# Optimization experiments

Measured on AMD Instinct MI355X. Metric: run time of the kernel, lower is better.

## Reference

```python
import jax, jax.numpy as jnp
import numpy as np

D_MODEL = 384; N_LAYER = 8; N_MELS = 80; D_STATE = 16; EXPAND = 2; D_CONV = 4
D_INNER = EXPAND * D_MODEL           # 768
DT_RANK = (D_MODEL + 15) // 16       # 24 ('auto')
B = 4; L = 512


def setup_inputs() -> dict:
    key = jax.random.key(0)
    ks = jax.random.split(key, 12)
    g = lambda k, shape, s=0.02: jax.random.normal(k, shape, dtype=jnp.float32) * s
    A_log = jnp.tile(jnp.log(jnp.arange(1, D_STATE + 1, dtype=jnp.float32))[None, None, :],
                     (N_LAYER, D_INNER, 1))
    return {
        "x": jax.random.normal(ks[0], (B, L, N_MELS), dtype=jnp.float32),
        "enc_output": jax.random.normal(ks[1], (B, L, D_MODEL), dtype=jnp.float32),
        "w_in": g(ks[2], (N_MELS, D_MODEL)),
        "b_in": jnp.zeros((D_MODEL,), jnp.float32),
        "ln_w": jnp.ones((N_LAYER, D_MODEL), jnp.float32),
        "inproj_w": g(ks[3], (N_LAYER, D_MODEL, 2 * D_INNER)),
        "conv_w": g(ks[4], (N_LAYER, D_INNER, D_CONV), 0.1),
        "conv_b": jnp.zeros((N_LAYER, D_INNER), jnp.float32),
        "xproj_w": g(ks[5], (N_LAYER, D_INNER, DT_RANK + 2 * D_STATE)),
        "dtproj_w": g(ks[6], (N_LAYER, DT_RANK, D_INNER), 0.1),
        "dtproj_b": g(ks[7], (N_LAYER, D_INNER), 0.1),
        "A_log": A_log,
        "D": jnp.ones((N_LAYER, D_INNER), jnp.float32),
        "outproj_w": g(ks[8], (N_LAYER, D_INNER, D_MODEL)),
        "normf_w": jnp.ones((D_MODEL,), jnp.float32),
        "w_out": g(ks[9], (D_MODEL, N_MELS)),
    }


def rmsnorm(x, w, eps=1e-5):
    return x * jax.lax.rsqrt(jnp.mean(x * x, axis=-1, keepdims=True) + eps) * w


def selective_scan(u, delta, A, Bm, Cm, Dp):
    # u, delta: (b,l,d); A: (d,n); Bm, Cm: (b,l,n); Dp: (d,)
    dA = jnp.exp(jnp.einsum('bld,dn->bldn', delta, A))          # (b,l,d,n)
    dBu = jnp.einsum('bld,bln,bld->bldn', delta, Bm, u)          # (b,l,d,n)

    def step(h, xs):
        dA_t, dBu_t, C_t = xs                                    # (b,d,n),(b,d,n),(b,n)
        h = dA_t * h + dBu_t
        y = jnp.einsum('bdn,bn->bd', h, C_t)
        return h, y

    h0 = jnp.zeros((u.shape[0], u.shape[2], A.shape[1]), u.dtype)
    _, ys = jax.lax.scan(step, h0, (dA.transpose(1, 0, 2, 3),
                                    dBu.transpose(1, 0, 2, 3),
                                    Cm.transpose(1, 0, 2)))
    return ys.transpose(1, 0, 2) + u * Dp                        # (b,l,d)


def mamba_layer(x, ln, ip, cw, cb, xp, dw, db, al, dp, op):
    h = rmsnorm(x, ln)
    xr = h @ ip                                                  # (b,l,2*d_inner)
    xs, res = jnp.split(xr, 2, axis=-1)
    # depthwise causal conv1d: pad d_conv-1 on the left, truncate to L
    xc = jax.lax.conv_general_dilated(xs.transpose(0, 2, 1), cw[:, None, :],
                                      (1,), [(D_CONV - 1, 0)],
                                      feature_group_count=D_INNER)
    xs = jax.nn.silu((xc + cb[None, :, None]).transpose(0, 2, 1))
    xdbl = xs @ xp                                               # (b,l,dt_rank+2n)
    dt = xdbl[..., :DT_RANK]
    Bm = xdbl[..., DT_RANK:DT_RANK + D_STATE]
    Cm = xdbl[..., DT_RANK + D_STATE:]
    delta = jax.nn.softplus(dt @ dw + db)
    y = selective_scan(xs, delta, -jnp.exp(al), Bm, Cm, dp)
    y = y * jax.nn.silu(res)
    return x + y @ op


def reference(x, enc_output, w_in, b_in, ln_w, inproj_w, conv_w, conv_b,
              xproj_w, dtproj_w, dtproj_b, A_log, D, outproj_w, normf_w, w_out):
    h = x @ w_in + b_in
    half = N_LAYER // 2
    for i in range(half):
        h = mamba_layer(h, ln_w[i], inproj_w[i], conv_w[i], conv_b[i], xproj_w[i],
                        dtproj_w[i], dtproj_b[i], A_log[i], D[i], outproj_w[i])
    # soft attention: decoder states attend over encoder output
    scores = jnp.einsum('bqd,bkd->bqk', h, enc_output)
    h = jnp.einsum('bqk,bkd->bqd', jax.nn.softmax(scores, axis=-1), enc_output)
    for i in range(half, N_LAYER):
        h = mamba_layer(h, ln_w[i], inproj_w[i], conv_w[i], conv_b[i], xproj_w[i],
                        dtproj_w[i], dtproj_b[i], A_log[i], D[i], outproj_w[i])
    h = rmsnorm(h, normf_w)
    return h @ w_out
```

## Files before the change

### kernel.cpp

```cpp
#include <hip/hip_runtime.h>
#include <hip/hip_bf16.h>
#include <math.h>

#define D_MODEL 384
#define N_LAYER 8
#define N_MELS  80
#define D_STATE 16
#define D_CONV  4
#define D_INNER 768
#define DT_RANK 24
#define BB      4
#define LL      512
#define MTOK    (BB*LL)

#define BMt 64
#define BNt 64
#define BKt 16

#define XP_N   56
#define XPS    12
#define XPKC   64

typedef __attribute__((ext_vector_type(8))) short bf16x8;
typedef __attribute__((ext_vector_type(4))) short bf16x4;
typedef __attribute__((ext_vector_type(4))) float f32x4;

__device__ __forceinline__ float silu_f(float x) { return x / (1.f + __expf(-x)); }
__device__ __forceinline__ short bf_raw(float x) {
  __hip_bfloat16 h = __float2bfloat16(x);
  return *reinterpret_cast<short*>(&h);
}
__device__ __forceinline__ float bfu(unsigned short u) {
  unsigned v = ((unsigned)u) << 16;
  return *reinterpret_cast<float*>(&v);
}

template<int EPI>
__global__ __launch_bounds__(256) void gemm_f32(
    const float* __restrict__ A, int lda,
    const float* __restrict__ W, int ldw,
    const float* __restrict__ bias,
    float* __restrict__ C, int ldc,
    int M, int N, int K)
{
  __shared__ float As[BKt][BMt];
  __shared__ float Ws[BKt][BNt];
  const int tid = threadIdx.x;
  const int tx = tid & 15, ty = tid >> 4;
  const int m0 = blockIdx.y * BMt, n0 = blockIdx.x * BNt;
  const int am = tid >> 2, ak4 = (tid & 3) << 2;
  const int wk = tid >> 4, wn4 = (tid & 15) << 2;

  float acc[4][4] = {};

  for (int k0 = 0; k0 < K; k0 += BKt) {
    float4 va = make_float4(0.f, 0.f, 0.f, 0.f);
    {
      int m = m0 + am;
      if (m < M) {
        if (k0 + ak4 + 3 < K) {
          va = *reinterpret_cast<const float4*>(&A[(size_t)m * lda + k0 + ak4]);
        } else {
          float t[4];
          #pragma unroll
          for (int j = 0; j < 4; ++j)
            t[j] = (k0 + ak4 + j < K) ? A[(size_t)m * lda + k0 + ak4 + j] : 0.f;
          va = make_float4(t[0], t[1], t[2], t[3]);
        }
      }
    }
    As[ak4 + 0][am] = va.x;
    As[ak4 + 1][am] = va.y;
    As[ak4 + 2][am] = va.z;
    As[ak4 + 3][am] = va.w;

    float4 vw = make_float4(0.f, 0.f, 0.f, 0.f);
    {
      int kw = k0 + wk;
      if (kw < K) {
        if (n0 + wn4 + 3 < N) {
          vw = *reinterpret_cast<const float4*>(&W[(size_t)kw * ldw + n0 + wn4]);
        } else {
          float t[4];
          #pragma unroll
          for (int j = 0; j < 4; ++j)
            t[j] = (n0 + wn4 + j < N) ? W[(size_t)kw * ldw + n0 + wn4 + j] : 0.f;
          vw = make_float4(t[0], t[1], t[2], t[3]);
        }
      }
    }
    *reinterpret_cast<float4*>(&Ws[wk][wn4]) = vw;

    __syncthreads();
    #pragma unroll
    for (int kk = 0; kk < BKt; ++kk) {
      const float4 a4 = *reinterpret_cast<const float4*>(&As[kk][ty << 2]);
      const float4 w4 = *reinterpret_cast<const float4*>(&Ws[kk][tx << 2]);
      float av[4] = {a4.x, a4.y, a4.z, a4.w};
      float wv[4] = {w4.x, w4.y, w4.z, w4.w};
      #pragma unroll
      for (int i = 0; i < 4; ++i)
        #pragma unroll
        for (int j = 0; j < 4; ++j)
          acc[i][j] += av[i] * wv[j];
    }
    __syncthreads();
  }

  #pragma unroll
  for (int i = 0; i < 4; ++i) {
    int row = m0 + (ty << 2) + i;
    if (row >= M) continue;
    #pragma unroll
    for (int j = 0; j < 4; ++j) {
      int col = n0 + (tx << 2) + j;
      if (col >= N) continue;
      float v = acc[i][j];
      if (EPI == 1) v += bias[col];
      C[(size_t)row * ldc + col] = v;
    }
  }
}

template<int EPI, int OBF>
__global__ __launch_bounds__(256) void gemm_bf16(
    const __hip_bfloat16* __restrict__ A,
    const __hip_bfloat16* __restrict__ WT,
    const float* __restrict__ resid,
    float* __restrict__ C,
    __hip_bfloat16* __restrict__ Cb,
    int ldc, int M, int N, int K)
{
  __shared__ __align__(16) __hip_bfloat16 Asl[64][72];
  __shared__ __align__(16) __hip_bfloat16 Bsl[64][72];
  const int tid = threadIdx.x;
  const int wave = tid >> 6, lane = tid & 63;
  const int m0 = blockIdx.y * 64, n0 = blockIdx.x * 64;
  const int lrow = tid >> 2;
  const int lk   = (tid & 3) << 4;
  const int g16 = lane >> 4;
  const int l16 = lane & 15;

  f32x4 acc[4] = {};

  for (int k0 = 0; k0 < K; k0 += 64) {
    const uint4* ga = reinterpret_cast<const uint4*>(&A[(size_t)(m0 + lrow) * K + k0 + lk]);
    uint4* la = reinterpret_cast<uint4*>(&Asl[lrow][lk]);
    la[0] = ga[0]; la[1] = ga[1];
    const uint4* gb = reinterpret_cast<const uint4*>(&WT[(size_t)(n0 + lrow) * K + k0 + lk]);
    uint4* lb = reinterpret_cast<uint4*>(&Bsl[lrow][lk]);
    lb[0] = gb[0]; lb[1] = gb[1];
    __syncthreads();
    #pragma unroll
    for (int kk = 0; kk < 64; kk += 32) {
      bf16x8 a = *reinterpret_cast<const bf16x8*>(&Asl[wave * 16 + l16][kk + g16 * 8]);
      #pragma unroll
      for (int f = 0; f < 4; ++f) {
        bf16x8 b = *reinterpret_cast<const bf16x8*>(&Bsl[f * 16 + l16][kk + g16 * 8]);
        acc[f] = __builtin_amdgcn_mfma_f32_16x16x32_bf16(a, b, acc[f], 0, 0, 0);
      }
    }
    __syncthreads();
  }

  #pragma unroll
  for (int f = 0; f < 4; ++f) {
    #pragma unroll
    for (int r = 0; r < 4; ++r) {
      int row = m0 + wave * 16 + g16 * 4 + r;
      int col = n0 + f * 16 + l16;
      float v = acc[f][r];
      if (EPI == 3) v += resid[(size_t)row * ldc + col];
      if (OBF) Cb[(size_t)row * ldc + col] = __float2bfloat16(v);
      else     C[(size_t)row * ldc + col] = v;
    }
  }
}

__global__ __launch_bounds__(256) void gemm_bf16_bat(
    const __hip_bfloat16* __restrict__ A, size_t sA,
    const __hip_bfloat16* __restrict__ WT, size_t sW,
    float* __restrict__ C, size_t sC,
    int M, int N, int K)
{
  A  += (size_t)blockIdx.z * sA;
  WT += (size_t)blockIdx.z * sW;
  C  += (size_t)blockIdx.z * sC;
  __shared__ __align__(16) __hip_bfloat16 Asl[64][72];
  __shared__ __align__(16) __hip_bfloat16 Bsl[64][72];
  const int tid = threadIdx.x;
  const int wave = tid >> 6, lane = tid & 63;
  const int m0 = blockIdx.y * 64, n0 = blockIdx.x * 64;
  const int lrow = tid >> 2;
  const int lk   = (tid & 3) << 4;
  const int g16 = lane >> 4;
  const int l16 = lane & 15;

  f32x4 acc[4] = {};

  for (int k0 = 0; k0 < K; k0 += 64) {
    const uint4* ga = reinterpret_cast<const uint4*>(&A[(size_t)(m0 + lrow) * K + k0 + lk]);
    uint4* la = reinterpret_cast<uint4*>(&Asl[lrow][lk]);
    la[0] = ga[0]; la[1] = ga[1];
    const uint4* gb = reinterpret_cast<const uint4*>(&WT[(size_t)(n0 + lrow) * K + k0 + lk]);
    uint4* lb = reinterpret_cast<uint4*>(&Bsl[lrow][lk]);
    lb[0] = gb[0]; lb[1] = gb[1];
    __syncthreads();
    #pragma unroll
    for (int kk = 0; kk < 64; kk += 32) {
      bf16x8 a = *reinterpret_cast<const bf16x8*>(&Asl[wave * 16 + l16][kk + g16 * 8]);
      #pragma unroll
      for (int f = 0; f < 4; ++f) {
        bf16x8 b = *reinterpret_cast<const bf16x8*>(&Bsl[f * 16 + l16][kk + g16 * 8]);
        acc[f] = __builtin_amdgcn_mfma_f32_16x16x32_bf16(a, b, acc[f], 0, 0, 0);
      }
    }
    __syncthreads();
  }

  #pragma unroll
  for (int f = 0; f < 4; ++f) {
    #pragma unroll
    for (int r = 0; r < 4; ++r) {
      int row = m0 + wave * 16 + g16 * 4 + r;
      int col = n0 + f * 16 + l16;
      C[(size_t)row * N + col] = acc[f][r];
    }
  }
}

__global__ __launch_bounds__(256) void xproj_conv_splitk(
    const __hip_bfloat16* __restrict__ xrb,
    const float* __restrict__ cw,
    const float* __restrict__ cb,
    const __hip_bfloat16* __restrict__ WT,
    float* __restrict__ part)
{
  __shared__ __align__(16) __hip_bfloat16 Asl[64][72];
  __shared__ __align__(16) __hip_bfloat16 Bsl[64][72];
  const int tid = threadIdx.x;
  const int wave = tid >> 6, lane = tid & 63;
  const int split = blockIdx.x;
  const int m0 = blockIdx.y * 64;
  const int kbase = split * XPKC;
  const int lrow = tid >> 2;
  const int lk   = (tid & 3) << 4;
  const int g16 = lane >> 4;
  const int l16 = lane & 15;

  {
    const int m = m0 + lrow;
    const int b = m >> 9, l = m & 511;
    const int dcol0 = kbase + lk;
    unsigned wrow[4][8];
    #pragma unroll
    for (int k = 0; k < 4; ++k) {
      int t = l - 3 + k;
      if (t >= 0) {
        const uint4* p = reinterpret_cast<const uint4*>(
            &xrb[((size_t)(b * LL + t)) * (2 * D_INNER) + dcol0]);
        uint4 q0 = p[0], q1 = p[1];
        wrow[k][0] = q0.x; wrow[k][1] = q0.y; wrow[k][2] = q0.z; wrow[k][3] = q0.w;
        wrow[k][4] = q1.x; wrow[k][5] = q1.y; wrow[k][6] = q1.z; wrow[k][7] = q1.w;
      } else {
        #pragma unroll
        for (int w = 0; w < 8; ++w) wrow[k][w] = 0u;
      }
    }
    #pragma unroll
    for (int j = 0; j < 16; ++j) {
      float4 cw4 = *reinterpret_cast<const float4*>(&cw[(size_t)(dcol0 + j) * 4]);
      float cwa[4] = {cw4.x, cw4.y, cw4.z, cw4.w};
      float a = cb[dcol0 + j];
      #pragma unroll
      for (int k = 0; k < 4; ++k) {
        unsigned w = wrow[k][j >> 1];
        unsigned short hv = (j & 1) ? (unsigned short)(w >> 16) : (unsigned short)(w & 0xffff);
        a += bfu(hv) * cwa[k];
      }
      Asl[lrow][lk + j] = __float2bfloat16(silu_f(a));
    }
  }

  const uint4* gb = reinterpret_cast<const uint4*>(&WT[(size_t)lrow * D_INNER + kbase + lk]);
  uint4* lb = reinterpret_cast<uint4*>(&Bsl[lrow][lk]);
  lb[0] = gb[0]; lb[1] = gb[1];
  __syncthreads();

  f32x4 acc[4] = {};
  #pragma unroll
  for (int kk = 0; kk < 64; kk += 32) {
    bf16x8 a = *reinterpret_cast<const bf16x8*>(&Asl[wave * 16 + l16][kk + g16 * 8]);
    #pragma unroll
    for (int f = 0; f < 4; ++f) {
      bf16x8 b = *reinterpret_cast<const bf16x8*>(&Bsl[f * 16 + l16][kk + g16 * 8]);
      acc[f] = __builtin_amdgcn_mfma_f32_16x16x32_bf16(a, b, acc[f], 0, 0, 0);
    }
  }

  #pragma unroll
  for (int f = 0; f < 4; ++f) {
    #pragma unroll
    for (int r = 0; r < 4; ++r) {
      int row = m0 + wave * 16 + g16 * 4 + r;
      int col = f * 16 + l16;
      part[((size_t)split * MTOK + row) * 64 + col] = acc[f][r];
    }
  }
}

__global__ __launch_bounds__(256) void xproj_reduce_kernel(
    const float* __restrict__ part, float* __restrict__ xdbl)
{
  int idx = blockIdx.x * 256 + threadIdx.x;
  if (idx >= MTOK * XP_N) return;
  int m = idx / XP_N, col = idx - m * XP_N;
  float s = 0.f;
  #pragma unroll
  for (int p = 0; p < XPS; ++p)
    s += part[((size_t)p * MTOK + m) * 64 + col];
  xdbl[idx] = s;
}

__global__ __launch_bounds__(256) void wconv_t_kernel(
    const float* __restrict__ src, __hip_bfloat16* __restrict__ dst,
    int K, int N, size_t ldl)
{
  __shared__ float tile[32][33];
  int l = blockIdx.z;
  int kb = blockIdx.y * 32, nb = blockIdx.x * 32;
  int tn = threadIdx.x & 31, tk = threadIdx.x >> 5;
  const float* s = src + (size_t)l * K * N;
  __hip_bfloat16* dd = dst + (size_t)l * ldl;
  #pragma unroll
  for (int i = 0; i < 4; ++i) {
    int k = kb + tk + i * 8, n = nb + tn;
    tile[tk + i * 8][tn] = (k < K && n < N) ? s[(size_t)k * N + n] : 0.f;
  }
  __syncthreads();
  #pragma unroll
  for (int i = 0; i < 4; ++i) {
    int n = nb + tk + i * 8, k = kb + tn;
    if (n < N && k < K) dd[(size_t)n * K + k] = __float2bfloat16(tile[tn][tk + i * 8]);
  }
}

__global__ __launch_bounds__(256) void f2b_kernel(
    const float* __restrict__ src, __hip_bfloat16* __restrict__ dst, int n)
{
  int i = (blockIdx.x * 256 + threadIdx.x) * 4;
  if (i >= n) return;
  float4 v = *reinterpret_cast<const float4*>(&src[i]);
  bf16x4 o;
  o[0] = bf_raw(v.x); o[1] = bf_raw(v.y); o[2] = bf_raw(v.z); o[3] = bf_raw(v.w);
  *reinterpret_cast<bf16x4*>(&dst[i]) = o;
}

__global__ __launch_bounds__(256) void softmax_rows_kernel(
    const float* __restrict__ scores, __hip_bfloat16* __restrict__ P)
{
  int row = (blockIdx.x * 256 + threadIdx.x) >> 6;
  int lane = threadIdx.x & 63;
  if (row >= BB * LL) return;
  const float* s = scores + (size_t)row * LL + lane * 8;
  float4 v0 = *reinterpret_cast<const float4*>(s);
  float4 v1 = *reinterpret_cast<const float4*>(s + 4);
  float mx = fmaxf(fmaxf(fmaxf(v0.x, v0.y), fmaxf(v0.z, v0.w)),
                   fmaxf(fmaxf(v1.x, v1.y), fmaxf(v1.z, v1.w)));
  #pragma unroll
  for (int off = 32; off; off >>= 1) mx = fmaxf(mx, __shfl_xor(mx, off, 64));
  float e[8];
  e[0] = __expf(v0.x - mx); e[1] = __expf(v0.y - mx);
  e[2] = __expf(v0.z - mx); e[3] = __expf(v0.w - mx);
  e[4] = __expf(v1.x - mx); e[5] = __expf(v1.y - mx);
  e[6] = __expf(v1.z - mx); e[7] = __expf(v1.w - mx);
  float sum = ((e[0] + e[1]) + (e[2] + e[3])) + ((e[4] + e[5]) + (e[6] + e[7]));
  #pragma unroll
  for (int off = 32; off; off >>= 1) sum += __shfl_xor(sum, off, 64);
  float inv = 1.f / sum;
  bf16x8 o;
  #pragma unroll
  for (int j = 0; j < 8; ++j) o[j] = bf_raw(e[j] * inv);
  *reinterpret_cast<bf16x8*>(&P[(size_t)row * LL + lane * 8]) = o;
}

__global__ __launch_bounds__(256) void rmsnorm_kernel(
    const float* __restrict__ x, const float* __restrict__ w,
    float* __restrict__ out, __hip_bfloat16* __restrict__ outb, int M, int N)
{
  int gw = (blockIdx.x * blockDim.x + threadIdx.x) >> 6;
  int lane = threadIdx.x & 63;
  if (gw >= M) return;
  const float* row = x + (size_t)gw * N;
  float ss = 0.f;
  for (int j = lane; j < N; j += 64) { float v = row[j]; ss += v * v; }
  #pragma unroll
  for (int off = 32; off; off >>= 1) ss += __shfl_xor(ss, off, 64);
  float scale = rsqrtf(ss / (float)N + 1e-5f);
  float* orow = out ? out + (size_t)gw * N : nullptr;
  __hip_bfloat16* brow = outb + (size_t)gw * N;
  for (int j = lane; j < N; j += 64) {
    float v = row[j] * scale * w[j];
    if (orow) orow[j] = v;
    brow[j] = __float2bfloat16(v);
  }
}

#define SC6_T  16
#define SC6_NC 32
__global__ __launch_bounds__(512) void scan_kernel10(
    const __hip_bfloat16* __restrict__ xrb,
    const float* __restrict__ xdbl,
    const float* __restrict__ A_log,
    const float* __restrict__ Dp,
    const float* __restrict__ dtw,
    const float* __restrict__ dtb,
    const float* __restrict__ cw,
    const float* __restrict__ cb,
    __hip_bfloat16* __restrict__ yg)
{
  __shared__ float sdelta[2][LL];
  __shared__ unsigned supk[LL];
  __shared__ float sdw[2][DT_RANK];
  __shared__ float sP[2][SC6_NC][D_STATE + 1];
  __shared__ float sS[2][SC6_NC][D_STATE + 1];
  __shared__ float sH0[2][SC6_NC][D_STATE + 1];
  __shared__ float sY[2][LL][5];

  unsigned* sxr = reinterpret_cast<unsigned*>(&sY[0][0][0]);

  const int id = blockIdx.x;
  const int r  = id / 48;
  const int G  = id % 48;
  const int b  = G / 12;
  const int q  = G % 12;
  const int d0 = q * 64 + 2 * r;
  const int d1 = d0 + 1;

  const int tid = threadIdx.x;
  const int n = tid & 15;
  const int c = tid >> 4;

  if (tid < DT_RANK) {
    sdw[0][tid] = dtw[tid * D_INNER + d0];
    sdw[1][tid] = dtw[tid * D_INNER + d1];
  }
  if (tid < 3) sxr[tid] = 0u;
  __syncthreads();

  {
    const int l = tid;
    const size_t m = (size_t)(b * LL + l);
    float acc0 = dtb[d0], acc1 = dtb[d1];
    const float* xrow = &xdbl[m * 56];
    #pragma unroll
    for (int k4 = 0; k4 < DT_RANK; k4 += 4) {
      float4 xv = *reinterpret_cast<const float4*>(&xrow[k4]);
      acc0 += xv.x * sdw[0][k4] + xv.y * sdw[0][k4 + 1] + xv.z * sdw[0][k4 + 2] + xv.w * sdw[0][k4 + 3];
      acc1 += xv.x * sdw[1][k4] + xv.y * sdw[1][k4 + 1] + xv.z * sdw[1][k4 + 2] + xv.w * sdw[1][k4 + 3];
    }
    sdelta[0][l] = (acc0 > 20.f) ? acc0 : log1pf(__expf(acc0));
    sdelta[1][l] = (acc1 > 20.f) ? acc1 : log1pf(__expf(acc1));
    sxr[3 + l] = *reinterpret_cast<const unsigned*>(&xrb[m * (2 * D_INNER) + d0]);
  }
  __syncthreads();

  {
    const int l = tid;
    float4 cw0 = *reinterpret_cast<const float4*>(&cw[(size_t)d0 * 4]);
    float4 cw1 = *reinterpret_cast<const float4*>(&cw[(size_t)d1 * 4]);
    float cwa0[4] = {cw0.x, cw0.y, cw0.z, cw0.w};
    float cwa1[4] = {cw1.x, cw1.y, cw1.z, cw1.w};
    float u0 = cb[d0], u1 = cb[d1];
    #pragma unroll
    for (int k = 0; k < 4; ++k) {
      unsigned w = sxr[l + k];
      u0 += bfu((unsigned short)(w & 0xffff)) * cwa0[k];
      u1 += bfu((unsigned short)(w >> 16)) * cwa1[k];
    }
    unsigned pk = ((unsigned)(unsigned short)bf_raw(silu_f(u0))) |
                  (((unsigned)(unsigned short)bf_raw(silu_f(u1))) << 16);
    supk[l] = pk;
  }

  const float Aval0 = -__expf(A_log[d0 * D_STATE + n]);
  const float Aval1 = -__expf(A_log[d1 * D_STATE + n]);
  const int l0 = c * SC6_T;
  const size_t mbase = (size_t)(b * LL + l0);

  float Bv_s[SC6_T];
  #pragma unroll
  for (int t = 0; t < SC6_T; ++t)
    Bv_s[t] = xdbl[(mbase + t) * 56 + DT_RANK + n];

  __syncthreads();

  float a_s[2][SC6_T];
  {
    float P0 = 1.f, S0 = 0.f, P1 = 1.f, S1 = 0.f;
    #pragma unroll
    for (int t = 0; t < SC6_T; ++t) {
      int l = l0 + t;
      unsigned uu = supk[l];
      float uv0 = bfu((unsigned short)(uu & 0xffff));
      float uv1 = bfu((unsigned short)(uu >> 16));
      float dv0 = sdelta[0][l];
      float dv1 = sdelta[1][l];
      float a0 = __expf(dv0 * Aval0);
      float a1 = __expf(dv1 * Aval1);
      P0 *= a0; S0 = a0 * S0 + (dv0 * Bv_s[t]) * uv0;
      P1 *= a1; S1 = a1 * S1 + (dv1 * Bv_s[t]) * uv1;
      a_s[0][t] = a0; a_s[1][t] = a1;
    }
    sP[0][c][n] = P0; sS[0][c][n] = S0;
    sP[1][c][n] = P1; sS[1][c][n] = S1;
  }

  float Cv_s[SC6_T];
  #pragma unroll
  for (int t = 0; t < SC6_T; ++t)
    Cv_s[t] = xdbl[(mbase + t) * 56 + DT_RANK + D_STATE + n];

  __syncthreads();

  {
    const int c2 = tid & 31;
    const int n2 = tid >> 5;
    #pragma unroll
    for (int dd = 0; dd < 2; ++dd) {
      float p = sP[dd][c2][n2];
      float s = sS[dd][c2][n2];
      #pragma unroll
      for (int k = 1; k <= 16; k <<= 1) {
        float pp = __shfl_up(p, k, 64);
        float sp = __shfl_up(s, k, 64);
        if (c2 >= k) { s = p * sp + s; p = p * pp; }
      }
      if (c2 == 0) sH0[dd][0][n2] = 0.f;
      if (c2 < 31) sH0[dd][c2 + 1][n2] = s;
    }
  }
  __syncthreads();

  {
    float h0 = sH0[0][c][n];
    float h1 = sH0[1][c][n];
    #pragma unroll
    for (int t = 0; t < SC6_T; ++t) {
      int l = l0 + t;
      unsigned uu = supk[l];
      float uv0 = bfu((unsigned short)(uu & 0xffff));
      float uv1 = bfu((unsigned short)(uu >> 16));
      float dv0 = sdelta[0][l];
      float dv1 = sdelta[1][l];
      h0 = a_s[0][t] * h0 + (dv0 * Bv_s[t]) * uv0;
      h1 = a_s[1][t] * h1 + (dv1 * Bv_s[t]) * uv1;
      float c0 = h0 * Cv_s[t];
      float c1 = h1 * Cv_s[t];
      c0 += __shfl_xor(c0, 1, 64); c0 += __shfl_xor(c0, 2, 64);
      c1 += __shfl_xor(c1, 1, 64); c1 += __shfl_xor(c1, 2, 64);
      if ((n & 3) == 0) { sY[0][l][n >> 2] = c0; sY[1][l][n >> 2] = c1; }
    }
  }
  __syncthreads();

  {
    const int l = tid;
    const size_t m = (size_t)(b * LL + l);
    unsigned uu = supk[l];
    float uv0 = bfu((unsigned short)(uu & 0xffff));
    float uv1 = bfu((unsigned short)(uu >> 16));
    float y0 = (sY[0][l][0] + sY[0][l][1]) + (sY[0][l][2] + sY[0][l][3]) + uv0 * Dp[d0];
    float y1 = (sY[1][l][0] + sY[1][l][1]) + (sY[1][l][2] + sY[1][l][3]) + uv1 * Dp[d1];
    unsigned rr = *reinterpret_cast<const unsigned*>(&xrb[m * (2 * D_INNER) + D_INNER + d0]);
    float r0 = bfu((unsigned short)(rr & 0xffff));
    float r1 = bfu((unsigned short)(rr >> 16));
    y0 *= silu_f(r0);
    y1 *= silu_f(r1);
    unsigned outw = ((unsigned)(unsigned short)bf_raw(y0)) |
                    (((unsigned)(unsigned short)bf_raw(y1)) << 16);
    *reinterpret_cast<unsigned*>(&yg[m * D_INNER + d0]) = outw;
  }
}

extern "C" void kernel_launch(void* const* d_in, const int* in_sizes, int n_in,
                              void* d_out, int out_size, void* d_ws, size_t ws_size,
                              hipStream_t stream) {
  const float* x        = (const float*)d_in[0];
  const float* enc      = (const float*)d_in[1];
  const float* w_in     = (const float*)d_in[2];
  const float* b_in     = (const float*)d_in[3];
  const float* ln_w     = (const float*)d_in[4];
  const float* inproj_w = (const float*)d_in[5];
  const float* conv_w   = (const float*)d_in[6];
  const float* conv_b   = (const float*)d_in[7];
  const float* xproj_w  = (const float*)d_in[8];
  const float* dtproj_w = (const float*)d_in[9];
  const float* dtproj_b = (const float*)d_in[10];
  const float* A_log    = (const float*)d_in[11];
  const float* Dvec     = (const float*)d_in[12];
  const float* outproj_w= (const float*)d_in[13];
  const float* normf_w  = (const float*)d_in[14];
  const float* w_out    = (const float*)d_in[15];

  float* ws = (float*)d_ws;
  float* h     = ws; ws += MTOK * D_MODEL;
  float* hn    = ws; ws += MTOK * D_MODEL;
  float* xdbl  = ws; ws += MTOK * XP_N;
  float* xpart = ws; ws += XPS * MTOK * 64;
  float* h2    = ws; ws += MTOK * D_MODEL;
  float* scores= ws; ws += BB * LL * LL;
  __hip_bfloat16* xr_bf = (__hip_bfloat16*)ws; ws += MTOK * 2 * D_INNER / 2;
  __hip_bfloat16* hn_bf = (__hip_bfloat16*)ws; ws += MTOK * D_MODEL / 2;
  __hip_bfloat16* yg_bf = (__hip_bfloat16*)ws; ws += MTOK * D_INNER / 2;
  __hip_bfloat16* h_bf  = (__hip_bfloat16*)ws; ws += MTOK * D_MODEL / 2;
  __hip_bfloat16* P_bf  = (__hip_bfloat16*)ws; ws += BB * LL * LL / 2;
  __hip_bfloat16* enc_bf= (__hip_bfloat16*)ws; ws += BB * LL * D_MODEL / 2;
  __hip_bfloat16* encT  = (__hip_bfloat16*)ws; ws += BB * LL * D_MODEL / 2;
  __hip_bfloat16* WinT  = (__hip_bfloat16*)ws; ws += N_LAYER * D_MODEL * 2 * D_INNER / 2;
  __hip_bfloat16* WoutT = (__hip_bfloat16*)ws; ws += N_LAYER * D_INNER * D_MODEL / 2;
  __hip_bfloat16* XpT   = (__hip_bfloat16*)ws; ws += N_LAYER * 64 * D_INNER / 2;

  dim3 blk256(256), blk512(512);

  wconv_t_kernel<<<dim3(2 * D_INNER / 32, D_MODEL / 32, N_LAYER), blk256, 0, stream>>>(
      inproj_w, WinT, D_MODEL, 2 * D_INNER, (size_t)2 * D_INNER * D_MODEL);
  wconv_t_kernel<<<dim3(D_MODEL / 32, D_INNER / 32, N_LAYER), blk256, 0, stream>>>(
      outproj_w, WoutT, D_INNER, D_MODEL, (size_t)D_MODEL * D_INNER);
  wconv_t_kernel<<<dim3((XP_N + 31) / 32, D_INNER / 32, N_LAYER), blk256, 0, stream>>>(
      xproj_w, XpT, D_INNER, XP_N, (size_t)64 * D_INNER);
  f2b_kernel<<<(BB * LL * D_MODEL / 4 + 255) / 256, blk256, 0, stream>>>(
      enc, enc_bf, BB * LL * D_MODEL);
  wconv_t_kernel<<<dim3(D_MODEL / 32, LL / 32, BB), blk256, 0, stream>>>(
      enc, encT, LL, D_MODEL, (size_t)D_MODEL * LL);

  gemm_f32<1><<<dim3(D_MODEL / BNt, MTOK / BMt), blk256, 0, stream>>>(
      x, N_MELS, w_in, D_MODEL, b_in, h, D_MODEL, MTOK, D_MODEL, N_MELS);

  auto mamba = [&](float* hcur, int i) {
    rmsnorm_kernel<<<MTOK * 64 / 256, blk256, 0, stream>>>(
        hcur, ln_w + (size_t)i * D_MODEL, nullptr, hn_bf, MTOK, D_MODEL);
    gemm_bf16<0, 1><<<dim3(2 * D_INNER / 64, MTOK / 64), blk256, 0, stream>>>(
        hn_bf, WinT + (size_t)i * D_MODEL * 2 * D_INNER, nullptr,
        nullptr, xr_bf, 2 * D_INNER, MTOK, 2 * D_INNER, D_MODEL);
    xproj_conv_splitk<<<dim3(XPS, MTOK / 64), blk256, 0, stream>>>(
        xr_bf, conv_w + (size_t)i * D_INNER * D_CONV, conv_b + (size_t)i * D_INNER,
        XpT + (size_t)i * 64 * D_INNER, xpart);
    xproj_reduce_kernel<<<(MTOK * XP_N + 255) / 256, blk256, 0, stream>>>(xpart, xdbl);
    scan_kernel10<<<BB * D_INNER / 2, blk512, 0, stream>>>(
        xr_bf, xdbl, A_log + (size_t)i * D_INNER * D_STATE, Dvec + (size_t)i * D_INNER,
        dtproj_w + (size_t)i * DT_RANK * D_INNER, dtproj_b + (size_t)i * D_INNER,
        conv_w + (size_t)i * D_INNER * D_CONV, conv_b + (size_t)i * D_INNER,
        yg_bf);
    gemm_bf16<3, 0><<<dim3(D_MODEL / 64, MTOK / 64), blk256, 0, stream>>>(
        yg_bf, WoutT + (size_t)i * D_INNER * D_MODEL, hcur,
        hcur, nullptr, D_MODEL, MTOK, D_MODEL, D_INNER);
  };

  for (int i = 0; i < N_LAYER / 2; ++i) mamba(h, i);

  f2b_kernel<<<(MTOK * D_MODEL / 4 + 255) / 256, blk256, 0, stream>>>(
      h, h_bf, MTOK * D_MODEL);
  gemm_bf16_bat<<<dim3(LL / 64, LL / 64, BB), blk256, 0, stream>>>(
      h_bf, (size_t)LL * D_MODEL, enc_bf, (size_t)LL * D_MODEL,
      scores, (size_t)LL * LL, LL, LL, D_MODEL);
  softmax_rows_kernel<<<(BB * LL * 64) / 256, blk256, 0, stream>>>(scores, P_bf);
  gemm_bf16_bat<<<dim3(D_MODEL / 64, LL / 64, BB), blk256, 0, stream>>>(
      P_bf, (size_t)LL * LL, encT, (size_t)D_MODEL * LL,
      h2, (size_t)LL * D_MODEL, LL, D_MODEL, LL);

  for (int i = N_LAYER / 2; i < N_LAYER; ++i) mamba(h2, i);

  rmsnorm_kernel<<<MTOK * 64 / 256, blk256, 0, stream>>>(h2, normf_w, hn, hn_bf, MTOK, D_MODEL);
  gemm_f32<0><<<dim3((N_MELS + BNt - 1) / BNt, MTOK / BMt), blk256, 0, stream>>>(
      hn, D_MODEL, w_out, N_MELS, nullptr, (float*)d_out, N_MELS, MTOK, N_MELS, D_MODEL);
}
```

Before: 714.0 us.

## Fuse RMSNorm into in-projection GEMM and emit bf16 copy from out-proj epilogue

Each Mamba layer's RMSNorm kernel is folded into a new in-projection GEMM. That GEMM computes per-row scales from fp32 h, then normalizes and converts to bf16 while staging A tiles in shared memory. The last pre-attention out-projection GEMM now writes both fp32 and bf16 outputs, which removes a separate f2b pass, and the final rmsnorm drops its unused bf16 output. This saves 8 norm launches and the hn_bf round-trip. The cost is that the fp32 H rows are re-read by each of the 24 column blocks, and the A-tile stores to shared memory become scalar bf16 writes.

Result: slower. 766.7 us (+7.4%).

```diff
diff --git a/kernel.cpp b/kernel.cpp
--- a/kernel.cpp
+++ b/kernel.cpp
@@ -171,8 +171,84 @@
       int col = n0 + f * 16 + l16;
       float v = acc[f][r];
       if (EPI == 3) v += resid[(size_t)row * ldc + col];
-      if (OBF) Cb[(size_t)row * ldc + col] = __float2bfloat16(v);
-      else     C[(size_t)row * ldc + col] = v;
+      if (OBF == 1) {
+        Cb[(size_t)row * ldc + col] = __float2bfloat16(v);
+      } else {
+        C[(size_t)row * ldc + col] = v;
+        if (OBF == 2) Cb[(size_t)row * ldc + col] = __float2bfloat16(v);
+      }
+    }
+  }
+}
+
+__global__ __launch_bounds__(256) void gemm_rms_inproj(
+    const float* __restrict__ H,
+    const float* __restrict__ lnw,
+    const __hip_bfloat16* __restrict__ WT,
+    __hip_bfloat16* __restrict__ Cb)
+{
+  __shared__ __align__(16) __hip_bfloat16 Asl[64][72];
+  __shared__ __align__(16) __hip_bfloat16 Bsl[64][72];
+  __shared__ float sscale[64];
+  const int tid = threadIdx.x;
+  const int wave = tid >> 6, lane = tid & 63;
+  const int m0 = blockIdx.y * 64, n0 = blockIdx.x * 64;
+  const int lrow = tid >> 2;
+  const int lk   = (tid & 3) << 4;
+  const int g16 = lane >> 4;
+  const int l16 = lane & 15;
+
+  {
+    const int sub = tid & 3;
+    const float* hrow = &H[(size_t)(m0 + lrow) * D_MODEL + sub * 96];
+    float ss = 0.f;
+    #pragma unroll
+    for (int j = 0; j < 96; j += 4) {
+      float4 v = *reinterpret_cast<const float4*>(&hrow[j]);
+      ss += v.x * v.x + v.y * v.y + v.z * v.z + v.w * v.w;
+    }
+    ss += __shfl_xor(ss, 1, 64);
+    ss += __shfl_xor(ss, 2, 64);
+    if (sub == 0) sscale[lrow] = rsqrtf(ss / (float)D_MODEL + 1e-5f);
+  }
+  __syncthreads();
+
+  f32x4 acc[4] = {};
+  const float sc = sscale[lrow];
+
+  for (int k0 = 0; k0 < D_MODEL; k0 += 64) {
+    #pragma unroll
+    for (int j = 0; j < 16; j += 4) {
+      float4 hv = *reinterpret_cast<const float4*>(&H[(size_t)(m0 + lrow) * D_MODEL + k0 + lk + j]);
+      float4 wv = *reinterpret_cast<const float4*>(&lnw[k0 + lk + j]);
+      Asl[lrow][lk + j + 0] = __float2bfloat16(hv.x * sc * wv.x);
+      Asl[lrow][lk + j + 1] = __float2bfloat16(hv.y * sc * wv.y);
+      Asl[lrow][lk + j + 2] = __float2bfloat16(hv.z * sc * wv.z);
+      Asl[lrow][lk + j + 3] = __float2bfloat16(hv.w * sc * wv.w);
+    }
+    const uint4* gb = reinterpret_cast<const uint4*>(&WT[(size_t)(n0 + lrow) * D_MODEL + k0 + lk]);
+    uint4* lb = reinterpret_cast<uint4*>(&Bsl[lrow][lk]);
+    lb[0] = gb[0]; lb[1] = gb[1];
+    __syncthreads();
+    #pragma unroll
+    for (int kk = 0; kk < 64; kk += 32) {
+      bf16x8 a = *reinterpret_cast<const bf16x8*>(&Asl[wave * 16 + l16][kk + g16 * 8]);
+      #pragma unroll
+      for (int f = 0; f < 4; ++f) {
+        bf16x8 b = *reinterpret_cast<const bf16x8*>(&Bsl[f * 16 + l16][kk + g16 * 8]);
+        acc[f] = __builtin_amdgcn_mfma_f32_16x16x32_bf16(a, b, acc[f], 0, 0, 0);
+      }
+    }
+    __syncthreads();
+  }
+
+  #pragma unroll
+  for (int f = 0; f < 4; ++f) {
+    #pragma unroll
+    for (int r = 0; r < 4; ++r) {
+      int row = m0 + wave * 16 + g16 * 4 + r;
+      int col = n0 + f * 16 + l16;
+      Cb[(size_t)row * (2 * D_INNER) + col] = __float2bfloat16(acc[f][r]);
     }
   }
 }
@@ -386,7 +462,7 @@
 
 __global__ __launch_bounds__(256) void rmsnorm_kernel(
     const float* __restrict__ x, const float* __restrict__ w,
-    float* __restrict__ out, __hip_bfloat16* __restrict__ outb, int M, int N)
+    float* __restrict__ out, int M, int N)
 {
   int gw = (blockIdx.x * blockDim.x + threadIdx.x) >> 6;
   int lane = threadIdx.x & 63;
@@ -397,13 +473,8 @@
   #pragma unroll
   for (int off = 32; off; off >>= 1) ss += __shfl_xor(ss, off, 64);
   float scale = rsqrtf(ss / (float)N + 1e-5f);
-  float* orow = out ? out + (size_t)gw * N : nullptr;
-  __hip_bfloat16* brow = outb + (size_t)gw * N;
-  for (int j = lane; j < N; j += 64) {
-    float v = row[j] * scale * w[j];
-    if (orow) orow[j] = v;
-    brow[j] = __float2bfloat16(v);
-  }
+  float* orow = out + (size_t)gw * N;
+  for (int j = lane; j < N; j += 64) orow[j] = row[j] * scale * w[j];
 }
 
 #define SC6_T  16
@@ -611,7 +682,6 @@
   float* h2    = ws; ws += MTOK * D_MODEL;
   float* scores= ws; ws += BB * LL * LL;
   __hip_bfloat16* xr_bf = (__hip_bfloat16*)ws; ws += MTOK * 2 * D_INNER / 2;
-  __hip_bfloat16* hn_bf = (__hip_bfloat16*)ws; ws += MTOK * D_MODEL / 2;
   __hip_bfloat16* yg_bf = (__hip_bfloat16*)ws; ws += MTOK * D_INNER / 2;
   __hip_bfloat16* h_bf  = (__hip_bfloat16*)ws; ws += MTOK * D_MODEL / 2;
   __hip_bfloat16* P_bf  = (__hip_bfloat16*)ws; ws += BB * LL * LL / 2;
@@ -637,12 +707,10 @@
   gemm_f32<1><<<dim3(D_MODEL / BNt, MTOK / BMt), blk256, 0, stream>>>(
       x, N_MELS, w_in, D_MODEL, b_in, h, D_MODEL, MTOK, D_MODEL, N_MELS);
 
-  auto mamba = [&](float* hcur, int i) {
-    rmsnorm_kernel<<<MTOK * 64 / 256, blk256, 0, stream>>>(
-        hcur, ln_w + (size_t)i * D_MODEL, nullptr, hn_bf, MTOK, D_MODEL);
-    gemm_bf16<0, 1><<<dim3(2 * D_INNER / 64, MTOK / 64), blk256, 0, stream>>>(
-        hn_bf, WinT + (size_t)i * D_MODEL * 2 * D_INNER, nullptr,
-        nullptr, xr_bf, 2 * D_INNER, MTOK, 2 * D_INNER, D_MODEL);
+  auto mamba = [&](float* hcur, int i, bool dualOut) {
+    gemm_rms_inproj<<<dim3(2 * D_INNER / 64, MTOK / 64), blk256, 0, stream>>>(
+        hcur, ln_w + (size_t)i * D_MODEL,
+        WinT + (size_t)i * D_MODEL * 2 * D_INNER, xr_bf);
     xproj_conv_splitk<<<dim3(XPS, MTOK / 64), blk256, 0, stream>>>(
         xr_bf, conv_w + (size_t)i * D_INNER * D_CONV, conv_b + (size_t)i * D_INNER,
         XpT + (size_t)i * 64 * D_INNER, xpart);
@@ -652,15 +720,18 @@
         dtproj_w + (size_t)i * DT_RANK * D_INNER, dtproj_b + (size_t)i * D_INNER,
         conv_w + (size_t)i * D_INNER * D_CONV, conv_b + (size_t)i * D_INNER,
         yg_bf);
-    gemm_bf16<3, 0><<<dim3(D_MODEL / 64, MTOK / 64), blk256, 0, stream>>>(
-        yg_bf, WoutT + (size_t)i * D_INNER * D_MODEL, hcur,
-        hcur, nullptr, D_MODEL, MTOK, D_MODEL, D_INNER);
+    if (dualOut)
+      gemm_bf16<3, 2><<<dim3(D_MODEL / 64, MTOK / 64), blk256, 0, stream>>>(
+          yg_bf, WoutT + (size_t)i * D_INNER * D_MODEL, hcur,
+          hcur, h_bf, D_MODEL, MTOK, D_MODEL, D_INNER);
+    else
+      gemm_bf16<3, 0><<<dim3(D_MODEL / 64, MTOK / 64), blk256, 0, stream>>>(
+          yg_bf, WoutT + (size_t)i * D_INNER * D_MODEL, hcur,
+          hcur, nullptr, D_MODEL, MTOK, D_MODEL, D_INNER);
   };
 
-  for (int i = 0; i < N_LAYER / 2; ++i) mamba(h, i);
-
-  f2b_kernel<<<(MTOK * D_MODEL / 4 + 255) / 256, blk256, 0, stream>>>(
-      h, h_bf, MTOK * D_MODEL);
+  for (int i = 0; i < N_LAYER / 2; ++i) mamba(h, i, i == N_LAYER / 2 - 1);
+
   gemm_bf16_bat<<<dim3(LL / 64, LL / 64, BB), blk256, 0, stream>>>(
       h_bf, (size_t)LL * D_MODEL, enc_bf, (size_t)LL * D_MODEL,
       scores, (size_t)LL * LL, LL, LL, D_MODEL);
@@ -669,9 +740,9 @@
       P_bf, (size_t)LL * LL, encT, (size_t)D_MODEL * LL,
       h2, (size_t)LL * D_MODEL, LL, D_MODEL, LL);
 
-  for (int i = N_LAYER / 2; i < N_LAYER; ++i) mamba(h2, i);
-
-  rmsnorm_kernel<<<MTOK * 64 / 256, blk256, 0, stream>>>(h2, normf_w, hn, hn_bf, MTOK, D_MODEL);
+  for (int i = N_LAYER / 2; i < N_LAYER; ++i) mamba(h2, i, false);
+
+  rmsnorm_kernel<<<MTOK * 64 / 256, blk256, 0, stream>>>(h2, normf_w, hn, MTOK, D_MODEL);
   gemm_f32<0><<<dim3((N_MELS + BNt - 1) / BNt, MTOK / BMt), blk256, 0, stream>>>(
       hn, D_MODEL, w_out, N_MELS, nullptr, (float*)d_out, N_MELS, MTOK, N_MELS, D_MODEL);
 }
```
